# Kernel optimization log

Measured on AMD Instinct MI355X. Metric: run time of the kernel, lower is better.

## Reference

```python
import jax, jax.numpy as jnp
import numpy as np

GROUP_SIZE = 128  # in_features // scales.shape[1]


def setup_inputs() -> dict:
    key = jax.random.key(0)
    kA, kq, ks, kz, kb = jax.random.split(key, 5)
    M, K, N = 2048, 4096, 4096
    G = K // GROUP_SIZE  # 32 groups
    A = jax.random.normal(kA, (M, K), dtype=jnp.float32)
    # unpacked uint4 quantized weights, values in [0, 16)
    qweight = jax.random.randint(kq, (N, K), 0, 16, dtype=jnp.int32)
    # per-group scales (typical GPTQ magnitude) and zero-points (float, 'original' zeros_mode)
    scales = jax.random.uniform(ks, (N, G), dtype=jnp.float32) * 0.02
    zeros = jax.random.uniform(kz, (N, G), dtype=jnp.float32) * 15.0
    bias = jax.random.normal(kb, (N,), dtype=jnp.float32)
    return {"A": A, "qweight": qweight, "scales": scales, "zeros": zeros, "bias": bias}


def reference(A, qweight, scales, zeros, bias):
    # Dequant: W[n,k] = (q[n,k] - zeros[n, k//gs]) * scales[n, k//gs]
    N, K = qweight.shape
    gs = K // scales.shape[1]
    s = jnp.repeat(scales, gs, axis=1)  # [N, K]
    z = jnp.repeat(zeros, gs, axis=1)   # [N, K]
    W = (qweight.astype(A.dtype) - z) * s
    # out[m,n] = sum_k A[m,k] * W[n,k] + bias[n]
    return jnp.einsum("mk,nk->mn", A, W) + bias
```

## Files before the change

### kernel.cpp

```cpp
#include <hip/hip_runtime.h>
#include <cstdint>
#include <cstddef>

#define MM 2048
#define KK 4096
#define NN 4096
#define GG 32
#define BM 128
#define BN 128
#define BK 64
#define NKT (KK / BK)

typedef _Float16 half8_t __attribute__((ext_vector_type(8)));
typedef _Float16 half4_t __attribute__((ext_vector_type(4)));
typedef float f32x4 __attribute__((ext_vector_type(4)));

__device__ __forceinline__ void load_lds16(const void* gptr, void* lptr) {
  __builtin_amdgcn_global_load_lds(
      (const __attribute__((address_space(1))) unsigned int*)gptr,
      (__attribute__((address_space(3))) unsigned int*)lptr, 16, 0, 0);
}

#define ACNT (MM * KK / 4)
__global__ void prep_kernel(const float* __restrict__ A, const int* __restrict__ q,
                            const float* __restrict__ scales, const float* __restrict__ zeros,
                            _Float16* __restrict__ Ah, _Float16* __restrict__ Wh) {
  const int i = blockIdx.x * blockDim.x + threadIdx.x;
  if (i < ACNT) {
    const float4 v = ((const float4*)A)[i];
    half4_t h;
    h[0] = (_Float16)v.x; h[1] = (_Float16)v.y; h[2] = (_Float16)v.z; h[3] = (_Float16)v.w;
    *(half4_t*)(Ah + 4 * (size_t)i) = h;
  } else {
    const int j = i - ACNT;
    const int e = j << 2;
    const int n = e >> 12;
    const int k = e & (KK - 1);
    const int g = k >> 7;
    const float sc = scales[(n << 5) + g];
    const float zp = zeros[(n << 5) + g];
    const float nzs = -zp * sc;
    const int4 qv = ((const int4*)q)[j];
    half4_t h;
    h[0] = (_Float16)fmaf((float)qv.x, sc, nzs);
    h[1] = (_Float16)fmaf((float)qv.y, sc, nzs);
    h[2] = (_Float16)fmaf((float)qv.z, sc, nzs);
    h[3] = (_Float16)fmaf((float)qv.w, sc, nzs);
    *(half4_t*)(Wh + (size_t)e) = h;
  }
}

__global__ __launch_bounds__(512, 4)
void gemm_pipe(const _Float16* __restrict__ Ah, const _Float16* __restrict__ Wh,
               const float* __restrict__ bias, float* __restrict__ out)
{
  __shared__ __align__(16) _Float16 sA[2][BM * BK];
  __shared__ __align__(16) _Float16 sB[2][BN * BK];
  __shared__ int flg[4];

  const int tid = threadIdx.x;
  const int lane = tid & 63;
  const int wave = tid >> 6;

  if (tid == 0) { flg[0] = 0; flg[1] = 0; flg[2] = 0; flg[3] = 0; }
  __syncthreads();

  const int bid = blockIdx.x;
  const int xcd = bid & 7;
  const int slot = bid >> 3;
  const int m0 = (slot >> 2) * BM;
  const int n0 = (xcd * 4 + (slot & 3)) * BN;

  if (wave >= 4) {
    const int pw = wave - 4;
    const int srow = lane >> 3;
    const int scc = lane & 7;
    const int gchunk = scc ^ srow;
    for (int t = 0; t < NKT; ++t) {
      const int b = t & 1;
      const int k0 = t * BK;
      const int need = 4 * (t >> 1);
      while (__hip_atomic_load(&flg[2 + b], __ATOMIC_ACQUIRE,
                               __HIP_MEMORY_SCOPE_WORKGROUP) < need)
        __builtin_amdgcn_s_sleep(1);
#pragma unroll
      for (int i = 0; i < 4; ++i) {
        const int c = i * 4 + pw;
        const int row = c * 8 + srow;
        load_lds16(Ah + (size_t)(m0 + row) * KK + k0 + gchunk * 8, (void*)&sA[b][c * 512]);
        load_lds16(Wh + (size_t)(n0 + row) * KK + k0 + gchunk * 8, (void*)&sB[b][c * 512]);
      }
      __builtin_amdgcn_s_waitcnt(0x0f70);
      if (lane == 0)
        __hip_atomic_fetch_add(&flg[b], 1, __ATOMIC_RELEASE,
                               __HIP_MEMORY_SCOPE_WORKGROUP);
    }
    return;
  }

  const int wr = wave >> 1, wc = wave & 1;
  const int lr = lane & 15, quad = lane >> 4;

  f32x4 acc[4][4];
#pragma unroll
  for (int i = 0; i < 4; ++i)
#pragma unroll
    for (int j = 0; j < 4; ++j) acc[i][j] = (f32x4){0.f, 0.f, 0.f, 0.f};

  for (int t = 0; t < NKT; ++t) {
    const int b = t & 1;
    const int need = 4 * ((t >> 1) + 1);
    while (__hip_atomic_load(&flg[b], __ATOMIC_ACQUIRE,
                             __HIP_MEMORY_SCOPE_WORKGROUP) < need)
      __builtin_amdgcn_s_sleep(1);
#pragma unroll
    for (int ks = 0; ks < 2; ++ks) {
      half8_t a[4], bfr[4];
#pragma unroll
      for (int tt = 0; tt < 4; ++tt) {
        const int rA = wr * 64 + tt * 16 + lr;
        const int j = ks * 4 + quad;
        a[tt] = *(const half8_t*)&sA[b][rA * 64 + ((j ^ (lr & 7)) * 8)];
        const int rB = wc * 64 + tt * 16 + lr;
        bfr[tt] = *(const half8_t*)&sB[b][rB * 64 + ((j ^ (lr & 7)) * 8)];
      }
#pragma unroll
      for (int mi = 0; mi < 4; ++mi)
#pragma unroll
        for (int ni = 0; ni < 4; ++ni)
          acc[mi][ni] = __builtin_amdgcn_mfma_f32_16x16x32_f16(a[mi], bfr[ni], acc[mi][ni], 0, 0, 0);
    }
    __builtin_amdgcn_s_waitcnt(0xc07f);
    if (lane == 0)
      __hip_atomic_fetch_add(&flg[2 + b], 1, __ATOMIC_RELEASE,
                             __HIP_MEMORY_SCOPE_WORKGROUP);
  }

#pragma unroll
  for (int ni = 0; ni < 4; ++ni) {
    const int n = n0 + wc * 64 + ni * 16 + lr;
    const float bv = bias[n];
#pragma unroll
    for (int mi = 0; mi < 4; ++mi) {
      const int mbase = m0 + wr * 64 + mi * 16 + quad * 4;
#pragma unroll
      for (int r = 0; r < 4; ++r)
        out[(size_t)(mbase + r) * NN + n] = acc[mi][ni][r] + bv;
    }
  }
}

__global__ __launch_bounds__(256, 2)
void gemm_fused(const float* __restrict__ Af, const int* __restrict__ qw,
                const float* __restrict__ scales, const float* __restrict__ zeros,
                const float* __restrict__ bias, float* __restrict__ out)
{
  __shared__ __align__(16) _Float16 sA[BM * BK];
  __shared__ __align__(16) _Float16 sB[BN * BK];
  const int tid = threadIdx.x;
  const int lane = tid & 63;
  const int wave = tid >> 6;
  const int wr = wave >> 1, wc = wave & 1;
  const int m0 = (blockIdx.x >> 5) * BM;
  const int n0 = (blockIdx.x & 31) * BN;
  const int lr = lane & 15, quad = lane >> 4;
  f32x4 acc[4][4];
#pragma unroll
  for (int i = 0; i < 4; ++i)
#pragma unroll
    for (int j = 0; j < 4; ++j) acc[i][j] = (f32x4){0.f, 0.f, 0.f, 0.f};
  const int frow = tid >> 4;
  const int fc4 = tid & 15;
  for (int kt = 0; kt < NKT; ++kt) {
    const int k0 = kt * BK;
    const int g = k0 >> 7;
#pragma unroll
    for (int p = 0; p < 8; ++p) {
      const int row = p * 16 + frow;
      const int pc = (fc4 >> 1) ^ (row & 7);
      const int dst = row * 64 + pc * 8 + (fc4 & 1) * 4;
      const float4 avf = *(const float4*)&Af[(size_t)(m0 + row) * KK + k0 + fc4 * 4];
      half4_t ah;
      ah[0] = (_Float16)avf.x; ah[1] = (_Float16)avf.y;
      ah[2] = (_Float16)avf.z; ah[3] = (_Float16)avf.w;
      *(half4_t*)&sA[dst] = ah;
      const int n = n0 + row;
      const float sc = scales[(n << 5) + g];
      const float zp = zeros[(n << 5) + g];
      const float nzs = -zp * sc;
      const int4 qv = *(const int4*)&qw[(size_t)n * KK + k0 + fc4 * 4];
      half4_t bh;
      bh[0] = (_Float16)fmaf((float)qv.x, sc, nzs);
      bh[1] = (_Float16)fmaf((float)qv.y, sc, nzs);
      bh[2] = (_Float16)fmaf((float)qv.z, sc, nzs);
      bh[3] = (_Float16)fmaf((float)qv.w, sc, nzs);
      *(half4_t*)&sB[dst] = bh;
    }
    __syncthreads();
#pragma unroll
    for (int ks = 0; ks < 2; ++ks) {
      half8_t a[4], bfr[4];
#pragma unroll
      for (int tt = 0; tt < 4; ++tt) {
        const int rA = wr * 64 + tt * 16 + lr;
        const int j = ks * 4 + quad;
        a[tt] = *(const half8_t*)&sA[rA * 64 + ((j ^ (lr & 7)) * 8)];
        const int rB = wc * 64 + tt * 16 + lr;
        bfr[tt] = *(const half8_t*)&sB[rB * 64 + ((j ^ (lr & 7)) * 8)];
      }
#pragma unroll
      for (int mi = 0; mi < 4; ++mi)
#pragma unroll
        for (int ni = 0; ni < 4; ++ni)
          acc[mi][ni] = __builtin_amdgcn_mfma_f32_16x16x32_f16(a[mi], bfr[ni], acc[mi][ni], 0, 0, 0);
    }
    __syncthreads();
  }
#pragma unroll
  for (int ni = 0; ni < 4; ++ni) {
    const int n = n0 + wc * 64 + ni * 16 + lr;
    const float bv = bias[n];
#pragma unroll
    for (int mi = 0; mi < 4; ++mi) {
      const int mbase = m0 + wr * 64 + mi * 16 + quad * 4;
#pragma unroll
      for (int r = 0; r < 4; ++r)
        out[(size_t)(mbase + r) * NN + n] = acc[mi][ni][r] + bv;
    }
  }
}

extern "C" void kernel_launch(void* const* d_in, const int* in_sizes, int n_in,
                              void* d_out, int out_size, void* d_ws, size_t ws_size,
                              hipStream_t stream) {
  (void)in_sizes; (void)n_in; (void)out_size;
  const float* A      = (const float*)d_in[0];
  const int*   qw     = (const int*)d_in[1];
  const float* scales = (const float*)d_in[2];
  const float* zeros  = (const float*)d_in[3];
  const float* bias   = (const float*)d_in[4];
  float* out = (float*)d_out;

  const size_t needA = (size_t)MM * KK * sizeof(_Float16);
  const size_t needW = (size_t)NN * KK * sizeof(_Float16);

  if (ws_size >= needA + needW) {
    _Float16* Ah = (_Float16*)d_ws;
    _Float16* Wh = (_Float16*)((char*)d_ws + needA);
    prep_kernel<<<((MM + NN) * KK / 4) / 256, 256, 0, stream>>>(A, qw, scales, zeros, Ah, Wh);
    gemm_pipe<<<dim3(NN / BN * MM / BM), dim3(512), 0, stream>>>(Ah, Wh, bias, out);
  } else {
    gemm_fused<<<dim3(NN / BN * MM / BM), dim3(256), 0, stream>>>(A, qw, scales, zeros, bias, out);
  }
}
```

Before: 205.9 us.

## Enlarge GEMM block tile to 256x128 and switch to 32x32x16 MFMA

Measured after the change: 212.4 us. 3.2% more time.

```diff
diff --git a/kernel.cpp b/kernel.cpp
--- a/kernel.cpp
+++ b/kernel.cpp
@@ -6,7 +6,7 @@
 #define KK 4096
 #define NN 4096
 #define GG 32
-#define BM 128
+#define BM 256
 #define BN 128
 #define BK 64
 #define NKT (KK / BK)
@@ -14,6 +14,7 @@
 typedef _Float16 half8_t __attribute__((ext_vector_type(8)));
 typedef _Float16 half4_t __attribute__((ext_vector_type(4)));
 typedef float f32x4 __attribute__((ext_vector_type(4)));
+typedef float f32x16 __attribute__((ext_vector_type(16)));
 
 __device__ __forceinline__ void load_lds16(const void* gptr, void* lptr) {
   __builtin_amdgcn_global_load_lds(
@@ -50,7 +51,7 @@
   }
 }
 
-__global__ __launch_bounds__(512, 4)
+__global__ __launch_bounds__(512, 2)
 void gemm_pipe(const _Float16* __restrict__ Ah, const _Float16* __restrict__ Wh,
                const float* __restrict__ bias, float* __restrict__ out)
 {
@@ -77,75 +78,90 @@
     const int scc = lane & 7;
     const int gchunk = scc ^ srow;
     for (int t = 0; t < NKT; ++t) {
-      const int b = t & 1;
+      const int bf = t & 1;
       const int k0 = t * BK;
       const int need = 4 * (t >> 1);
-      while (__hip_atomic_load(&flg[2 + b], __ATOMIC_ACQUIRE,
+      while (__hip_atomic_load(&flg[2 + bf], __ATOMIC_ACQUIRE,
                                __HIP_MEMORY_SCOPE_WORKGROUP) < need)
         __builtin_amdgcn_s_sleep(1);
 #pragma unroll
+      for (int i = 0; i < 8; ++i) {
+        const int c = pw + i * 4;
+        const int row = c * 8 + srow;
+        load_lds16(Ah + (size_t)(m0 + row) * KK + k0 + gchunk * 8, (void*)&sA[bf][c * 512]);
+      }
+#pragma unroll
       for (int i = 0; i < 4; ++i) {
-        const int c = i * 4 + pw;
+        const int c = pw + i * 4;
         const int row = c * 8 + srow;
-        load_lds16(Ah + (size_t)(m0 + row) * KK + k0 + gchunk * 8, (void*)&sA[b][c * 512]);
-        load_lds16(Wh + (size_t)(n0 + row) * KK + k0 + gchunk * 8, (void*)&sB[b][c * 512]);
+        load_lds16(Wh + (size_t)(n0 + row) * KK + k0 + gchunk * 8, (void*)&sB[bf][c * 512]);
       }
       __builtin_amdgcn_s_waitcnt(0x0f70);
       if (lane == 0)
-        __hip_atomic_fetch_add(&flg[b], 1, __ATOMIC_RELEASE,
+        __hip_atomic_fetch_add(&flg[bf], 1, __ATOMIC_RELEASE,
                                __HIP_MEMORY_SCOPE_WORKGROUP);
     }
     return;
   }
 
-  const int wr = wave >> 1, wc = wave & 1;
-  const int lr = lane & 15, quad = lane >> 4;
-
-  f32x4 acc[4][4];
+  const int wm = wave >> 1;
+  const int wn = wave & 1;
+  const int col = lane & 31;
+  const int khalf = lane >> 5;
+  const int l7 = lane & 7;
+
+  f32x16 acc[4][2];
 #pragma unroll
   for (int i = 0; i < 4; ++i)
 #pragma unroll
-    for (int j = 0; j < 4; ++j) acc[i][j] = (f32x4){0.f, 0.f, 0.f, 0.f};
+    for (int j = 0; j < 2; ++j)
+#pragma unroll
+      for (int r = 0; r < 16; ++r) acc[i][j][r] = 0.f;
 
   for (int t = 0; t < NKT; ++t) {
-    const int b = t & 1;
+    const int bf = t & 1;
     const int need = 4 * ((t >> 1) + 1);
-    while (__hip_atomic_load(&flg[b], __ATOMIC_ACQUIRE,
+    while (__hip_atomic_load(&flg[bf], __ATOMIC_ACQUIRE,
                              __HIP_MEMORY_SCOPE_WORKGROUP) < need)
       __builtin_amdgcn_s_sleep(1);
 #pragma unroll
-    for (int ks = 0; ks < 2; ++ks) {
-      half8_t a[4], bfr[4];
-#pragma unroll
-      for (int tt = 0; tt < 4; ++tt) {
-        const int rA = wr * 64 + tt * 16 + lr;
-        const int j = ks * 4 + quad;
-        a[tt] = *(const half8_t*)&sA[b][rA * 64 + ((j ^ (lr & 7)) * 8)];
-        const int rB = wc * 64 + tt * 16 + lr;
-        bfr[tt] = *(const half8_t*)&sB[b][rB * 64 + ((j ^ (lr & 7)) * 8)];
+    for (int ks = 0; ks < 4; ++ks) {
+      const int c = ks * 2 + khalf;
+      half8_t a[4], fb[2];
+#pragma unroll
+      for (int mi = 0; mi < 4; ++mi) {
+        const int row = wm * 128 + mi * 32 + col;
+        a[mi] = *(const half8_t*)&sA[bf][row * 64 + ((c ^ l7) * 8)];
+      }
+#pragma unroll
+      for (int ni = 0; ni < 2; ++ni) {
+        const int row = wn * 64 + ni * 32 + col;
+        fb[ni] = *(const half8_t*)&sB[bf][row * 64 + ((c ^ l7) * 8)];
       }
 #pragma unroll
       for (int mi = 0; mi < 4; ++mi)
 #pragma unroll
-        for (int ni = 0; ni < 4; ++ni)
-          acc[mi][ni] = __builtin_amdgcn_mfma_f32_16x16x32_f16(a[mi], bfr[ni], acc[mi][ni], 0, 0, 0);
+        for (int ni = 0; ni < 2; ++ni)
+          acc[mi][ni] = __builtin_amdgcn_mfma_f32_32x32x16_f16(a[mi], fb[ni], acc[mi][ni], 0, 0, 0);
     }
     __builtin_amdgcn_s_waitcnt(0xc07f);
     if (lane == 0)
-      __hip_atomic_fetch_add(&flg[2 + b], 1, __ATOMIC_RELEASE,
+      __hip_atomic_fetch_add(&flg[2 + bf], 1, __ATOMIC_RELEASE,
                              __HIP_MEMORY_SCOPE_WORKGROUP);
   }
 
 #pragma unroll
-  for (int ni = 0; ni < 4; ++ni) {
-    const int n = n0 + wc * 64 + ni * 16 + lr;
+  for (int ni = 0; ni < 2; ++ni) {
+    const int n = n0 + wn * 64 + ni * 32 + col;
     const float bv = bias[n];
 #pragma unroll
     for (int mi = 0; mi < 4; ++mi) {
-      const int mbase = m0 + wr * 64 + mi * 16 + quad * 4;
-#pragma unroll
-      for (int r = 0; r < 4; ++r)
-        out[(size_t)(mbase + r) * NN + n] = acc[mi][ni][r] + bv;
+      const int mb = m0 + wm * 128 + mi * 32 + 4 * khalf;
+#pragma unroll
+      for (int r = 0; r < 16; ++r) {
+        const int mrow = mb + (r & 3) + 8 * (r >> 2);
+        out[(size_t)mrow * NN + n] = acc[mi][ni][r] + bv;
+      }
     }
   }
 }
@@ -155,14 +171,14 @@
                 const float* __restrict__ scales, const float* __restrict__ zeros,
                 const float* __restrict__ bias, float* __restrict__ out)
 {
-  __shared__ __align__(16) _Float16 sA[BM * BK];
-  __shared__ __align__(16) _Float16 sB[BN * BK];
+  __shared__ __align__(16) _Float16 sA[128 * BK];
+  __shared__ __align__(16) _Float16 sB[128 * BK];
   const int tid = threadIdx.x;
   const int lane = tid & 63;
   const int wave = tid >> 6;
   const int wr = wave >> 1, wc = wave & 1;
-  const int m0 = (blockIdx.x >> 5) * BM;
-  const int n0 = (blockIdx.x & 31) * BN;
+  const int m0 = (blockIdx.x >> 5) * 128;
+  const int n0 = (blockIdx.x & 31) * 128;
   const int lr = lane & 15, quad = lane >> 4;
   f32x4 acc[4][4];
 #pragma unroll
@@ -248,8 +264,8 @@
     _Float16* Ah = (_Float16*)d_ws;
     _Float16* Wh = (_Float16*)((char*)d_ws + needA);
     prep_kernel<<<((MM + NN) * KK / 4) / 256, 256, 0, stream>>>(A, qw, scales, zeros, Ah, Wh);
-    gemm_pipe<<<dim3(NN / BN * MM / BM), dim3(512), 0, stream>>>(Ah, Wh, bias, out);
+    gemm_pipe<<<dim3((MM / BM) * (NN / BN)), dim3(512), 0, stream>>>(Ah, Wh, bias, out);
   } else {
-    gemm_fused<<<dim3(NN / BN * MM / BM), dim3(256), 0, stream>>>(A, qw, scales, zeros, bias, out);
-  }
-}
+    gemm_fused<<<dim3(512), dim3(256), 0, stream>>>(A, qw, scales, zeros, bias, out);
+  }
+}
```
